# Kernel optimization log

Hardware: AMD Instinct MI355X
Metric: run time of the kernel (lower is better)

## Reference

```python
import jax, jax.numpy as jnp
import numpy as np

N = 100000
E = 800000
D_IN = 128
D_OUT = 128
EPS = 1e-5


def setup_inputs() -> dict:
    key = jax.random.key(0)
    k = jax.random.split(key, 7)
    x = jax.random.normal(k[0], (N, D_IN), dtype=jnp.float32)
    edge_index = jax.random.randint(k[1], (2, E), 0, N, dtype=jnp.int64)
    # kaiming_uniform(a=sqrt(5)) on [out,in] -> bound = 1/sqrt(in_dim)
    bound = 1.0 / np.sqrt(D_IN)
    W_self = jax.random.uniform(k[2], (D_OUT, D_IN), minval=-bound, maxval=bound, dtype=jnp.float32)
    W_neigh = jax.random.uniform(k[3], (D_OUT, D_IN), minval=-bound, maxval=bound, dtype=jnp.float32)
    bias = jnp.zeros((D_OUT,), dtype=jnp.float32)
    gamma = jnp.ones((D_OUT,), dtype=jnp.float32)
    beta = jnp.zeros((D_OUT,), dtype=jnp.float32)
    return {"x": x, "edge_index": edge_index, "W_self": W_self,
            "W_neigh": W_neigh, "bias": bias, "gamma": gamma, "beta": beta}


def reference(x, edge_index, W_self, W_neigh, bias, gamma, beta):
    src, dst = edge_index[0], edge_index[1]
    # mean neighbor aggregation: segment-sum of gathered features / clamped degree
    agg = jax.ops.segment_sum(x[src], dst, num_segments=N)          # [N, D_IN]
    deg = jax.ops.segment_sum(jnp.ones_like(dst, dtype=x.dtype), dst, num_segments=N)
    neigh_mean = agg / jnp.maximum(deg, 1.0)[:, None]
    # dual linear + bias + ReLU
    out = jnp.einsum('nd,od->no', x, W_self) + jnp.einsum('nd,od->no', neigh_mean, W_neigh) + bias
    h = jax.nn.relu(out)
    # LayerNorm over last dim
    mu = jnp.mean(h, axis=-1, keepdims=True)
    var = jnp.var(h, axis=-1, keepdims=True)
    return (h - mu) * jax.lax.rsqrt(var + EPS) * gamma + beta
```

## Files before the change

kernel.cpp:

```cpp
#include <hip/hip_runtime.h>
#include <hip/hip_bf16.h>

#define N_NODES 100000
#define E_EDGES 800000
#define CAP 32
#define LN_EPS 1e-5f
#define WPAD 264
#define NX4 3200000

typedef __attribute__((ext_vector_type(4))) float f32x4;
typedef __attribute__((ext_vector_type(8))) short short8;

__device__ __forceinline__ unsigned short f2bf(float f) {
    __hip_bfloat16 h = __float2bfloat16(f);
    return *reinterpret_cast<unsigned short*>(&h);
}
__device__ __forceinline__ float bflo(unsigned int u) { return __uint_as_float(u << 16); }
__device__ __forceinline__ float bfhi(unsigned int u) { return __uint_as_float(u & 0xffff0000u); }

__global__ __launch_bounds__(256) void prep_kernel(
    const float* __restrict__ x, const int* __restrict__ ei,
    unsigned short* __restrict__ xb, int* __restrict__ cnt,
    int* __restrict__ slots)
{
    int i = blockIdx.x * blockDim.x + threadIdx.x;
    if (i < NX4) {
        float4 v = reinterpret_cast<const float4*>(x)[i];
        ushort4 o;
        o.x = f2bf(v.x); o.y = f2bf(v.y); o.z = f2bf(v.z); o.w = f2bf(v.w);
        reinterpret_cast<ushort4*>(xb)[i] = o;
    } else {
        int e = i - NX4;
        if (e >= E_EDGES) return;
        int src = ei[e];
        int dst = ei[E_EDGES + e];
        int p = atomicAdd(&cnt[dst], 1);
        if (p < CAP) slots[dst * CAP + p] = src;
    }
}

__global__ __launch_bounds__(256) void gather_kernel(
    const unsigned short* __restrict__ xb, const int* __restrict__ cnt,
    const int* __restrict__ slots, unsigned short* __restrict__ nb)
{
    int node = (blockIdx.x * blockDim.x + threadIdx.x) >> 6;
    int lane = threadIdx.x & 63;
    if (node >= N_NODES) return;
    int c = cnt[node];
    int cc = c > CAP ? CAP : c;
    int myslot = (lane < cc) ? slots[node * CAP + lane] : 0;
    const int subi = lane >> 4, chunk = lane & 15;
    float acc[8];
#pragma unroll
    for (int k = 0; k < 8; ++k) acc[k] = 0.f;
    const uint4* x4 = reinterpret_cast<const uint4*>(xb);
    for (int i = 0; i < cc; i += 4) {
        int idx = i + subi;
        int s = __shfl(myslot, idx);
        uint4 v = x4[s * 16 + chunk];
        if (idx < cc) {
            acc[0] += bflo(v.x); acc[1] += bfhi(v.x);
            acc[2] += bflo(v.y); acc[3] += bfhi(v.y);
            acc[4] += bflo(v.z); acc[5] += bfhi(v.z);
            acc[6] += bflo(v.w); acc[7] += bfhi(v.w);
        }
    }
#pragma unroll
    for (int k = 0; k < 8; ++k) {
        acc[k] += __shfl_xor(acc[k], 16);
        acc[k] += __shfl_xor(acc[k], 32);
    }
    if (subi == 0) {
        float inv = 1.0f / (float)(c > 1 ? c : 1);
        uint4 o;
        o.x = ((unsigned)f2bf(acc[1] * inv) << 16) | f2bf(acc[0] * inv);
        o.y = ((unsigned)f2bf(acc[3] * inv) << 16) | f2bf(acc[2] * inv);
        o.z = ((unsigned)f2bf(acc[5] * inv) << 16) | f2bf(acc[4] * inv);
        o.w = ((unsigned)f2bf(acc[7] * inv) << 16) | f2bf(acc[6] * inv);
        reinterpret_cast<uint4*>(nb)[node * 16 + chunk] = o;
    }
}

__global__ __launch_bounds__(256, 2) void fused_mfma(
    const unsigned short* __restrict__ xb, const unsigned short* __restrict__ nb,
    const float* __restrict__ Wself, const float* __restrict__ Wneigh,
    const float* __restrict__ bias, const float* __restrict__ gamma,
    const float* __restrict__ beta, float* __restrict__ out)
{
    __shared__ unsigned short WT[128][WPAD];
    const int t = threadIdx.x;
    const float4* Ws4 = reinterpret_cast<const float4*>(Wself);
    const float4* Wn4 = reinterpret_cast<const float4*>(Wneigh);
    for (int idx = t; idx < 4096; idx += 256) {
        int n = idx >> 5, k4 = (idx & 31) << 2;
        float4 a = Ws4[idx];
        float4 b = Wn4[idx];
        ushort4 ua, ub;
        ua.x = f2bf(a.x); ua.y = f2bf(a.y); ua.z = f2bf(a.z); ua.w = f2bf(a.w);
        ub.x = f2bf(b.x); ub.y = f2bf(b.y); ub.z = f2bf(b.z); ub.w = f2bf(b.w);
        *reinterpret_cast<ushort4*>(&WT[n][k4]) = ua;
        *reinterpret_cast<ushort4*>(&WT[n][128 + k4]) = ub;
    }
    __syncthreads();

    const int lane = t & 63, wave = t >> 6;
    const int l16 = lane & 15, quad = lane >> 4;
    float bia[8], gam[8], bet[8];
#pragma unroll
    for (int n = 0; n < 8; ++n) {
        int col = n * 16 + l16;
        bia[n] = bias[col]; gam[n] = gamma[col]; bet[n] = beta[col];
    }

    const int ntiles = (N_NODES + 255) / 256;
    for (int tile = blockIdx.x; tile < ntiles; tile += gridDim.x) {
        const int rowbase = tile * 256 + wave * 64;
        f32x4 acc[4][8];
#pragma unroll
        for (int m = 0; m < 4; ++m)
#pragma unroll
            for (int n = 0; n < 8; ++n) acc[m][n] = (f32x4)0.f;
        int rows[4];
#pragma unroll
        for (int m = 0; m < 4; ++m) {
            int r = rowbase + m * 16 + l16;
            rows[m] = r < N_NODES ? r : N_NODES - 1;
        }
#pragma unroll
        for (int kstep = 0; kstep < 8; ++kstep) {
            const unsigned short* Asrc = (kstep < 4) ? xb : nb;
            const int koff = (kstep & 3) * 32 + quad * 8;
            short8 a[4];
#pragma unroll
            for (int m = 0; m < 4; ++m)
                a[m] = *reinterpret_cast<const short8*>(Asrc + rows[m] * 128 + koff);
#pragma unroll
            for (int n = 0; n < 8; ++n) {
                short8 b = *reinterpret_cast<const short8*>(&WT[n * 16 + l16][kstep * 32 + quad * 8]);
#pragma unroll
                for (int m = 0; m < 4; ++m)
                    acc[m][n] = __builtin_amdgcn_mfma_f32_16x16x32_bf16(a[m], b, acc[m][n], 0, 0, 0);
            }
        }
#pragma unroll
        for (int m = 0; m < 4; ++m) {
#pragma unroll
            for (int r = 0; r < 4; ++r) {
                float h[8], s = 0.f, q = 0.f;
#pragma unroll
                for (int n = 0; n < 8; ++n) {
                    float v = acc[m][n][r] + bia[n];
                    v = fmaxf(v, 0.f);
                    h[n] = v; s += v; q += v * v;
                }
#pragma unroll
                for (int msk = 1; msk <= 8; msk <<= 1) {
                    s += __shfl_xor(s, msk);
                    q += __shfl_xor(q, msk);
                }
                const float mu = s * (1.f / 128.f);
                const float var = q * (1.f / 128.f) - mu * mu;
                const float rs = rsqrtf(var + LN_EPS);
                const int R = rowbase + m * 16 + quad * 4 + r;
                if (R < N_NODES) {
#pragma unroll
                    for (int n = 0; n < 8; ++n)
                        out[R * 128 + n * 16 + l16] = (h[n] - mu) * rs * gam[n] + bet[n];
                }
            }
        }
    }
}

extern "C" void kernel_launch(void* const* d_in, const int* in_sizes, int n_in,
                              void* d_out, int out_size, void* d_ws, size_t ws_size,
                              hipStream_t stream) {
    const float* x      = (const float*)d_in[0];
    const int*   ei     = (const int*)d_in[1];
    const float* Wself  = (const float*)d_in[2];
    const float* Wneigh = (const float*)d_in[3];
    const float* bias   = (const float*)d_in[4];
    const float* gamma  = (const float*)d_in[5];
    const float* beta   = (const float*)d_in[6];
    float* out = (float*)d_out;

    char* ws = (char*)d_ws;
    int* cnt   = (int*)ws;
    int* slots = (int*)(ws + 400000);
    unsigned short* xb  = (unsigned short*)(ws + 13200000);
    unsigned short* nb  = (unsigned short*)(ws + 38800000);

    hipMemsetAsync(cnt, 0, N_NODES * sizeof(int), stream);
    prep_kernel<<<(NX4 + E_EDGES + 255) / 256, 256, 0, stream>>>(x, ei, xb, cnt, slots);
    gather_kernel<<<(N_NODES + 3) / 4, 256, 0, stream>>>(xb, cnt, slots, nb);
    const int ntiles = (N_NODES + 255) / 256;
    fused_mfma<<<ntiles, 256, 0, stream>>>(xb, nb, Wself, Wneigh, bias, gamma, beta, out);
}
```

Baseline: 219.0 us.

## Bucket edges per node slice in shared memory, drop memset and global atomics

Replaces the flat prep kernel with 256 blocks that each own a slice of 391 destination nodes. Every block scans the full dst array, builds counts and slot lists with shared-memory atomics, and writes them out contiguously. The same blocks also convert their share of x to bf16, with odd and even blocks doing the two phases in opposite order. This removes the memset and the scattered global atomics, but each block now reads all 3.2MB of dst indices, and only 256 blocks run with heavy shared memory use.

```diff
diff --git a/kernel.cpp b/kernel.cpp
--- a/kernel.cpp
+++ b/kernel.cpp
@@ -6,7 +6,9 @@
 #define CAP 32
 #define LN_EPS 1e-5f
 #define WPAD 264
-#define NX4 3200000
+#define NSLICE 391
+#define SCAN4 200000
+#define CONV_PER_BLOCK 12500
 
 typedef __attribute__((ext_vector_type(4))) float f32x4;
 typedef __attribute__((ext_vector_type(8))) short short8;
@@ -18,25 +20,50 @@
 __device__ __forceinline__ float bflo(unsigned int u) { return __uint_as_float(u << 16); }
 __device__ __forceinline__ float bfhi(unsigned int u) { return __uint_as_float(u & 0xffff0000u); }
 
-__global__ __launch_bounds__(256) void prep_kernel(
+__global__ __launch_bounds__(256) void fill_slice(
     const float* __restrict__ x, const int* __restrict__ ei,
     unsigned short* __restrict__ xb, int* __restrict__ cnt,
     int* __restrict__ slots)
 {
-    int i = blockIdx.x * blockDim.x + threadIdx.x;
-    if (i < NX4) {
-        float4 v = reinterpret_cast<const float4*>(x)[i];
-        ushort4 o;
-        o.x = f2bf(v.x); o.y = f2bf(v.y); o.z = f2bf(v.z); o.w = f2bf(v.w);
-        reinterpret_cast<ushort4*>(xb)[i] = o;
-    } else {
-        int e = i - NX4;
-        if (e >= E_EDGES) return;
-        int src = ei[e];
-        int dst = ei[E_EDGES + e];
-        int p = atomicAdd(&cnt[dst], 1);
-        if (p < CAP) slots[dst * CAP + p] = src;
-    }
+    __shared__ int cnt_l[NSLICE];
+    __shared__ int slots_l[NSLICE * CAP];
+    const int t = threadIdx.x, b = blockIdx.x;
+    const int base = b * NSLICE;
+    for (int i = t; i < NSLICE; i += 256) cnt_l[i] = 0;
+    __syncthreads();
+
+    auto do_convert = [&]() {
+        const float4* x4 = reinterpret_cast<const float4*>(x);
+        ushort4* xb4 = reinterpret_cast<ushort4*>(xb);
+        const int j0 = b * CONV_PER_BLOCK;
+        for (int j = t; j < CONV_PER_BLOCK; j += 256) {
+            float4 v = x4[j0 + j];
+            ushort4 o;
+            o.x = f2bf(v.x); o.y = f2bf(v.y); o.z = f2bf(v.z); o.w = f2bf(v.w);
+            xb4[j0 + j] = o;
+        }
+    };
+    auto do_scan = [&]() {
+        const int4* d4 = reinterpret_cast<const int4*>(ei + E_EDGES);
+        for (int g = t; g < SCAN4; g += 256) {
+            int4 d = d4[g];
+#pragma unroll
+            for (int k = 0; k < 4; ++k) {
+                int dst = (k == 0) ? d.x : (k == 1) ? d.y : (k == 2) ? d.z : d.w;
+                unsigned lo = (unsigned)(dst - base);
+                if (lo < NSLICE) {
+                    int src = ei[4 * g + k];
+                    int p = atomicAdd(&cnt_l[lo], 1);
+                    if (p < CAP) slots_l[lo * CAP + p] = src;
+                }
+            }
+        }
+    };
+    if (b & 1) { do_convert(); do_scan(); }
+    else       { do_scan(); do_convert(); }
+    __syncthreads();
+    for (int i = t; i < NSLICE; i += 256) cnt[base + i] = cnt_l[i];
+    for (int i = t; i < NSLICE * CAP; i += 256) slots[base * CAP + i] = slots_l[i];
 }
 
 __global__ __launch_bounds__(256) void gather_kernel(
@@ -186,12 +213,11 @@
 
     char* ws = (char*)d_ws;
     int* cnt   = (int*)ws;
-    int* slots = (int*)(ws + 400000);
-    unsigned short* xb  = (unsigned short*)(ws + 13200000);
-    unsigned short* nb  = (unsigned short*)(ws + 38800000);
-
-    hipMemsetAsync(cnt, 0, N_NODES * sizeof(int), stream);
-    prep_kernel<<<(NX4 + E_EDGES + 255) / 256, 256, 0, stream>>>(x, ei, xb, cnt, slots);
+    int* slots = (int*)(ws + 400384);
+    unsigned short* xb  = (unsigned short*)(ws + 13212672);
+    unsigned short* nb  = (unsigned short*)(ws + 38812672);
+
+    fill_slice<<<256, 256, 0, stream>>>(x, ei, xb, cnt, slots);
     gather_kernel<<<(N_NODES + 3) / 4, 256, 0, stream>>>(xb, cnt, slots, nb);
     const int ntiles = (N_NODES + 255) / 256;
     fused_mfma<<<ntiles, 256, 0, stream>>>(xb, nb, Wself, Wneigh, bias, gamma, beta, out);
```

New measurement: 512.8 us. 134% more time.
